# Kernel optimization log

Hardware: AMD Instinct MI355X
Metric: run time of the kernel (lower is better)

## Reference

```python
import jax, jax.numpy as jnp
import numpy as np

E = 256        # HP.EMBED_SIZE
R = 8          # number of derivation rules / MLPs
S = 512        # number of sequential derivation steps
N = 256        # nodes produced per step
N_INIT = 1024  # initial axiom (thax) embeddings
TOTAL = N_INIT + S * N  # 132096 rows in the vectors buffer
M = 65536      # masked nodes fed to eval_net


def setup_inputs() -> dict:
    key = jax.random.key(0)
    ks = jax.random.split(key, 12)
    rng = np.random.default_rng(0)

    init_vecs = jax.random.normal(ks[0], (N_INIT, E), jnp.float32)
    # rule MLPs: concat(2 parents) -> E (relu) -> E
    W1 = jax.random.normal(ks[1], (R, 2 * E, E), jnp.float32) * (1.0 / np.sqrt(2 * E))
    b1 = jnp.zeros((R, E), jnp.float32)
    W2 = jax.random.normal(ks[2], (R, E, E), jnp.float32) * (1.0 / np.sqrt(E))
    b2 = jnp.zeros((R, E), jnp.float32)
    # eval net: E -> E (relu) -> 1
    eval_W1 = jax.random.normal(ks[3], (E, E), jnp.float32) * (1.0 / np.sqrt(E))
    eval_b1 = jnp.zeros((E,), jnp.float32)
    eval_W2 = jax.random.normal(ks[4], (E, 1), jnp.float32) * (1.0 / np.sqrt(E))
    eval_b2 = jnp.zeros((1,), jnp.float32)

    # step s writes rows [N_INIT + s*N, N_INIT + (s+1)*N)
    ind_steps = (N_INIT + np.arange(S * N, dtype=np.int32)).reshape(S, N)
    # parents drawn causally from already-computed prefix [0, N_INIT + s*N)
    highs = (N_INIT + np.arange(S, dtype=np.int64) * N)[:, None, None]
    pars_ind_steps = (rng.random((S, N, 2)) * highs).astype(np.int32)
    rule_steps = rng.integers(0, R, size=(S,)).astype(np.int32)
    mask = rng.integers(0, TOTAL, size=(M,)).astype(np.int32)

    pos = jax.random.uniform(ks[5], (M,), jnp.float32)
    neg = jax.random.uniform(ks[6], (M,), jnp.float32)
    target = jnp.round(jax.random.uniform(ks[7], (M,), jnp.float32))

    return {
        'init_vecs': init_vecs, 'W1': W1, 'b1': b1, 'W2': W2, 'b2': b2,
        'eval_W1': eval_W1, 'eval_b1': eval_b1, 'eval_W2': eval_W2, 'eval_b2': eval_b2,
        'pos': pos, 'neg': neg, 'target': target,
        'ind_steps': jnp.asarray(ind_steps), 'pars_ind_steps': jnp.asarray(pars_ind_steps),
        'rule_steps': jnp.asarray(rule_steps), 'mask': jnp.asarray(mask),
    }


def reference(init_vecs, W1, b1, W2, b2, eval_W1, eval_b1, eval_W2, eval_b2,
              pos, neg, target, ind_steps, pars_ind_steps, rule_steps, mask):
    vectors = jnp.zeros((TOTAL, E), init_vecs.dtype).at[:N_INIT].set(init_vecs)

    def step(vec, xs):
        inds, pars, r = xs            # [N], [N,2], scalar rule id
        p = vec[pars].reshape(N, 2 * E)   # gather parents
        h = jax.nn.relu(p @ W1[r] + b1[r])
        out = h @ W2[r] + b2[r]
        return vec.at[inds].set(out), None  # scatter new node embeddings

    vectors, _ = jax.lax.scan(step, vectors, (ind_steps, pars_ind_steps, rule_steps))

    x = vectors[mask]
    val = (jax.nn.relu(x @ eval_W1 + eval_b1) @ eval_W2 + eval_b2)[:, 0]

    # pos_weight = POS_WEIGHT_EXTRA * tot_neg / tot_pos (constant w.r.t. grads)
    pw = jax.lax.stop_gradient(jnp.sum(neg) / jnp.maximum(jnp.sum(pos), 1.0))
    # BCEWithLogitsLoss(pos_weight, reduction='none')
    contrib = pw * target * jax.nn.softplus(-val) + (1.0 - target) * jax.nn.softplus(val)
    loss = jnp.sum((pos + neg) * contrib)
    posOK = jnp.sum(pos * (val >= 0))
    negOK = jnp.sum(neg * (val < 0))
    return loss, posOK, negOK
```

## Files before the change

### kernel.cpp

```cpp
#include <hip/hip_runtime.h>
#include <math.h>

#define EMB   256
#define TWOE  512
#define NINIT 1024
#define NSTEP 512
#define NPS   256
#define TOTAL (NINIT + NSTEP * NPS)
#define MM    65536
#define NNODE (NSTEP * NPS)
#define NKEY  2048
#define BTH   512
#define TROWS 64
#define CHK_SH  16384
#define RULE_SH (24 * CHK_SH)

typedef short s16x8 __attribute__((ext_vector_type(8)));
typedef float f32x4 __attribute__((ext_vector_type(4)));

#define OFF_VECH   0ull
#define OFF_VECL   ((size_t)TOTAL * EMB * 2)
#define OFF_VAL    (2ull * (size_t)TOTAL * EMB * 2)
#define OFF_CNT    (OFF_VAL + (size_t)MM * 4)
#define OFF_ACC    (OFF_CNT + 4096)
#define OFF_PW     (OFF_ACC + 64)
#define OFF_KCNT   (OFF_PW + 192)
#define OFF_KOFS   (OFF_KCNT + (size_t)NKEY * 4)
#define OFF_NL     (OFF_KOFS + (size_t)NKEY * 4)
#define OFF_BROWS  (OFF_NL + 256)
#define OFF_LVL8   (OFF_BROWS + (size_t)NNODE * 4)
#define OFF_WSPLIT (OFF_LVL8 + 132352)


__device__ __forceinline__ void store_dev_u32(unsigned* p, unsigned v) {
  asm volatile("global_store_dword %0, %1, off sc0 sc1" :: "v"(p), "v"(v) : "memory");
}
__device__ __forceinline__ void store_dev_b64(void* p, uint2 v) {
  asm volatile("global_store_dwordx2 %0, %1, off sc0 sc1" :: "v"(p), "v"(v) : "memory");
}
__device__ __forceinline__ void store_dev_b128(void* p, uint4 v) {
  store_dev_b64(p, make_uint2(v.x, v.y));
  store_dev_b64((char*)p + 8, make_uint2(v.z, v.w));
}
__device__ __forceinline__ unsigned load_dev_u32(const unsigned* p) {
  unsigned r;
  asm volatile("global_load_dword %0, %1, off sc0 sc1\n\ts_waitcnt vmcnt(0)"
               : "=v"(r) : "v"(p) : "memory");
  return r;
}

__device__ __forceinline__ void gbar_tree(unsigned* cnt, int xcd) {
  asm volatile("s_waitcnt vmcnt(0)" ::: "memory");
  __syncthreads();
  if (threadIdx.x == 0) {
    unsigned* xarr = cnt + 32 * xcd;
    unsigned* garr = cnt + 512;
    unsigned* gep  = cnt + 544;
    unsigned* xep  = cnt + 576 + 32 * xcd;
    unsigned o = __hip_atomic_fetch_add(xarr, 1u, __ATOMIC_RELAXED, __HIP_MEMORY_SCOPE_AGENT);
    unsigned tgt = o / 32u + 1u;
    if ((o & 31u) == 31u) {
      unsigned g = __hip_atomic_fetch_add(garr, 1u, __ATOMIC_RELAXED, __HIP_MEMORY_SCOPE_AGENT);
      unsigned gt = g / 8u + 1u;
      if ((g & 7u) == 7u) store_dev_u32(gep, gt);
      else while (load_dev_u32(gep) < gt) __builtin_amdgcn_s_sleep(1);
      store_dev_u32(xep, tgt);
    } else {
      while (load_dev_u32(xep) < tgt) __builtin_amdgcn_s_sleep(1);
    }
  }
  __syncthreads();
}

__device__ __forceinline__ void split8(const float* f, uint4& h4, uint4& l4) {
  unsigned hu[8], lu[8];
  #pragma unroll
  for (int i = 0; i < 8; ++i) {
    unsigned u = __builtin_bit_cast(unsigned, f[i]);
    float rh = __builtin_bit_cast(float, u & 0xffff0000u);
    float rl = f[i] - rh;
    hu[i] = u >> 16;
    lu[i] = __builtin_bit_cast(unsigned, rl) >> 16;
  }
  h4 = make_uint4(hu[0] | (hu[1] << 16), hu[2] | (hu[3] << 16),
                  hu[4] | (hu[5] << 16), hu[6] | (hu[7] << 16));
  l4 = make_uint4(lu[0] | (lu[1] << 16), lu[2] | (lu[3] << 16),
                  lu[4] | (lu[5] << 16), lu[6] | (lu[7] << 16));
}

__device__ __forceinline__ void stage_chunk(short* ldst, const short* gsrc,
                                            int w, int lane) {
  #pragma unroll
  for (int i = 0; i < 4; ++i) {
    int off = (w * 4 + i) * 512;
    __builtin_amdgcn_global_load_lds(
        (const __attribute__((address_space(1))) unsigned int*)(gsrc + off + lane * 8),
        (__attribute__((address_space(3))) unsigned int*)(ldst + off), 16, 0, 0);
  }
}

__global__ void zero_scratch(unsigned* cnt, double* acc) {
  for (int i = threadIdx.x; i < 1024; i += 256) cnt[i] = 0u;
  if (threadIdx.x < 8) acc[threadIdx.x] = 0.0;
}

__global__ void init_convert(const float* __restrict__ src,
                             unsigned short* __restrict__ vh,
                             unsigned short* __restrict__ vl) {
  int slot = blockIdx.x * blockDim.x + threadIdx.x;
  float f[8];
  *(float4*)&f[0] = reinterpret_cast<const float4*>(src)[slot * 2];
  *(float4*)&f[4] = reinterpret_cast<const float4*>(src)[slot * 2 + 1];
  uint4 h4, l4;
  split8(f, h4, l4);
  *(uint4*)(vh + (size_t)slot * 8) = h4;
  *(uint4*)(vl + (size_t)slot * 8) = l4;
}

__global__ __launch_bounds__(512)
void presplit(const float* __restrict__ W1, const float* __restrict__ W2,
              short* __restrict__ Ws)
{
  const int blk = blockIdx.x;
  const int r = blk / 24, c = blk % 24;
  const float* src; int kbase;
  if (c < 16) { src = W1 + (size_t)r * TWOE * EMB; kbase = c * 32; }
  else        { src = W2 + (size_t)r * EMB * EMB;  kbase = (c - 16) * 32; }
  short* dst = Ws + (size_t)blk * CHK_SH;
  const int tid = threadIdx.x;
  #pragma unroll
  for (int u = 0; u < 2; ++u) {
    int qq = tid + u * 512;
    int g = qq >> 6, l = qq & 63;
    const float* p = src + (size_t)(kbase + ((l >> 4) << 3)) * EMB + (g << 4) + (l & 15);
    float f[8];
    #pragma unroll
    for (int i = 0; i < 8; ++i) f[i] = p[i * EMB];
    uint4 h4, l4;
    split8(f, h4, l4);
    *(uint4*)(dst + (size_t)qq * 8) = h4;
    *(uint4*)(dst + 8192 + (size_t)qq * 8) = l4;
  }
}

__global__ __launch_bounds__(256)
void prepass_levels(const int* __restrict__ pars, unsigned char* __restrict__ lvl8,
                    int* __restrict__ nlp)
{
  __shared__ unsigned char slvl[TOTAL];
  __shared__ int swmax[4];
  const int t = threadIdx.x;
  for (int i = t; i < NINIT; i += 256) slvl[i] = 0;
  __syncthreads();
  int Pa[8], Pb[8];
  #pragma unroll
  for (int w = 0; w < 8; ++w) {
    Pa[w] = pars[2 * (w * NPS + t)];
    Pb[w] = pars[2 * (w * NPS + t) + 1];
  }
  int lmax = 0;
  for (int s0 = 0; s0 < NSTEP; s0 += 8) {
    int Na[8], Nb[8];
    if (s0 + 8 < NSTEP) {
      #pragma unroll
      for (int w = 0; w < 8; ++w) {
        Na[w] = pars[2 * ((s0 + 8 + w) * NPS + t)];
        Nb[w] = pars[2 * ((s0 + 8 + w) * NPS + t) + 1];
      }
    } else {
      #pragma unroll
      for (int w = 0; w < 8; ++w) { Na[w] = 0; Nb[w] = 0; }
    }
    #pragma unroll
    for (int w = 0; w < 8; ++w) {
      int l1 = slvl[Pa[w]], l2 = slvl[Pb[w]];
      int lv = 1 + (l1 > l2 ? l1 : l2);
      slvl[NINIT + (s0 + w) * NPS + t] = (unsigned char)lv;
      if (lv > lmax) lmax = lv;
      __syncthreads();
    }
    #pragma unroll
    for (int w = 0; w < 8; ++w) { Pa[w] = Na[w]; Pb[w] = Nb[w]; }
  }
  const unsigned* sv = (const unsigned*)slvl;
  unsigned* gv = (unsigned*)lvl8;
  for (int i = t; i < TOTAL / 4; i += 256) gv[i] = sv[i];
  for (int o = 32; o; o >>= 1) lmax = max(lmax, __shfl_down(lmax, o));
  if ((t & 63) == 0) swmax[t >> 6] = lmax;
  __syncthreads();
  if (t == 0) {
    int m = 0;
    for (int w = 0; w < 4; ++w) m = max(m, swmax[w]);
    nlp[0] = m;
  }
}

__global__ __launch_bounds__(1024)
void prepass_bucket(const unsigned char* __restrict__ lvl8, const int* __restrict__ rules,
                    int* __restrict__ kcnt, int* __restrict__ kofs,
                    int* __restrict__ brows)
{
  __shared__ int scnt[NKEY];
  __shared__ int sofs[NKEY];
  const int t = threadIdx.x;
  for (int k = t; k < NKEY; k += 1024) scnt[k] = 0;
  __syncthreads();
  for (int i = t; i < NNODE; i += 1024) {
    int key = (int)lvl8[NINIT + i] * 8 + rules[i >> 8];
    atomicAdd(&scnt[key], 1);
  }
  __syncthreads();
  if (t == 0) {
    int run = 0;
    for (int k = 0; k < NKEY; ++k) {
      sofs[k] = run; kofs[k] = run; kcnt[k] = scnt[k]; run += scnt[k];
    }
  }
  __syncthreads();
  for (int i = t; i < NNODE; i += 1024) {
    int key = (int)lvl8[NINIT + i] * 8 + rules[i >> 8];
    int pos = atomicAdd(&sofs[key], 1);
    brows[pos] = i;
  }
}

__global__ __launch_bounds__(BTH, 1)
void scan_kernel(const short* __restrict__ Ws, const float* __restrict__ b1,
                 const float* __restrict__ b2, const int* __restrict__ pars,
                 unsigned short* __restrict__ vech, unsigned short* __restrict__ vecl,
                 const int* __restrict__ kcnt, const int* __restrict__ kofs,
                 const int* __restrict__ brows, const int* __restrict__ nlp,
                 unsigned* __restrict__ cnt)
{
  __shared__ short wB[2][CHK_SH];
  __shared__ float hL[TROWS][260];
  __shared__ int spar[2 * TROWS];
  __shared__ int sorow[TROWS];
  const int tid = threadIdx.x;
  const int bid = blockIdx.x;
  const int lane = tid & 63;
  const int w = tid >> 6;
  const int rw = w & 1, cwb = (w >> 1) << 2;
  const int row16 = lane & 15, kb8 = (lane >> 4) << 3;
  const int arow0 = (rw << 5) + row16;
  const int arow1 = arow0 + 16;
  const int hrow = (rw << 5) + ((lane >> 4) << 2);
  const int NL = nlp[0];
  const int xcd = bid & 7, jb = bid >> 3;

  for (int lv = 1; lv <= NL; ++lv) {
    int cum[9]; cum[0] = 0;
    int cnts[8], ofss[8];
    #pragma unroll
    for (int r = 0; r < 8; ++r) {
      int c = kcnt[lv * 8 + r];
      cnts[r] = c; ofss[r] = kofs[lv * 8 + r];
      cum[r + 1] = cum[r] + ((c + TROWS - 1) >> 6);
    }
    const int G = cum[8];
    const int q = G >> 3, rm = G & 7;
    const int Gx = q + (xcd < rm ? 1 : 0);
    const int sx = xcd * q + (xcd < rm ? xcd : rm);
    for (int j = jb; j < Gx; j += 32) {
      const int g = sx + j;
      int rr = 0;
      while (g >= cum[rr + 1]) ++rr;
      const int t0 = g - cum[rr];
      const int cnt_b = cnts[rr], ofs_b = ofss[rr];
      const int tbase = t0 * TROWS;
      const short* __restrict__ Wr = Ws + (size_t)rr * RULE_SH;

      __syncthreads();
      stage_chunk(&wB[0][0], Wr, w, lane);
      if (tid < 2 * TROWS) {
        int slot = tbase + (tid >> 1);
        if (slot >= cnt_b) slot = cnt_b - 1;
        int node = brows[ofs_b + slot];
        spar[tid] = pars[2 * node + (tid & 1)];
        if ((tid & 1) == 0) sorow[tid >> 1] = NINIT + node;
      }
      __syncthreads();
      const int p00 = spar[2 * arow0], p01 = spar[2 * arow0 + 1];
      const int p10 = spar[2 * arow1], p11 = spar[2 * arow1 + 1];
      float b1v[4], b2v[4];
      #pragma unroll
      for (int g4 = 0; g4 < 4; ++g4) {
        b1v[g4] = b1[rr * EMB + ((cwb + g4) << 4) + row16];
        b2v[g4] = b2[rr * EMB + ((cwb + g4) << 4) + row16];
      }
      uint4 a0h, a0l, a1h, a1l;
      {
        size_t o0 = (size_t)p00 * EMB + kb8;
        size_t o1 = (size_t)p10 * EMB + kb8;
        a0h = *(const uint4*)(vech + o0); a0l = *(const uint4*)(vecl + o0);
        a1h = *(const uint4*)(vech + o1); a1l = *(const uint4*)(vecl + o1);
      }
      asm volatile("s_waitcnt vmcnt(0)" ::: "memory");
      __syncthreads();
      f32x4 acc0[4] = {{0,0,0,0},{0,0,0,0},{0,0,0,0},{0,0,0,0}};
      f32x4 acc1[4] = {{0,0,0,0},{0,0,0,0},{0,0,0,0},{0,0,0,0}};
      int cur = 0;
      #pragma unroll
      for (int c = 0; c < 16; ++c) {
        stage_chunk(&wB[cur ^ 1][0], Wr + (size_t)(c + 1) * CHK_SH, w, lane);
        uint4 n0h, n0l, n1h, n1l;
        if (c < 15) {
          int kg = (c + 1) * 32 + kb8;
          int q0 = (kg >> 8) ? p01 : p00;
          int q1 = (kg >> 8) ? p11 : p10;
          size_t o0 = (size_t)q0 * EMB + (kg & 255);
          size_t o1 = (size_t)q1 * EMB + (kg & 255);
          n0h = *(const uint4*)(vech + o0); n0l = *(const uint4*)(vecl + o0);
          n1h = *(const uint4*)(vech + o1); n1l = *(const uint4*)(vecl + o1);
        }
        s16x8 A0h = __builtin_bit_cast(s16x8, a0h);
        s16x8 A0l = __builtin_bit_cast(s16x8, a0l);
        s16x8 A1h = __builtin_bit_cast(s16x8, a1h);
        s16x8 A1l = __builtin_bit_cast(s16x8, a1l);
        #pragma unroll
        for (int g4 = 0; g4 < 4; ++g4) {
          const short* bp = &wB[cur][((cwb + g4) * 64 + lane) * 8];
          s16x8 Bh = *(const s16x8*)bp;
          s16x8 Bl = *(const s16x8*)(bp + 8192);
          acc0[g4] = __builtin_amdgcn_mfma_f32_16x16x32_bf16(A0h, Bh, acc0[g4], 0, 0, 0);
          acc0[g4] = __builtin_amdgcn_mfma_f32_16x16x32_bf16(A0h, Bl, acc0[g4], 0, 0, 0);
          acc0[g4] = __builtin_amdgcn_mfma_f32_16x16x32_bf16(A0l, Bh, acc0[g4], 0, 0, 0);
          acc1[g4] = __builtin_amdgcn_mfma_f32_16x16x32_bf16(A1h, Bh, acc1[g4], 0, 0, 0);
          acc1[g4] = __builtin_amdgcn_mfma_f32_16x16x32_bf16(A1h, Bl, acc1[g4], 0, 0, 0);
          acc1[g4] = __builtin_amdgcn_mfma_f32_16x16x32_bf16(A1l, Bh, acc1[g4], 0, 0, 0);
        }
        if (c == 15) {
          #pragma unroll
          for (int g4 = 0; g4 < 4; ++g4) {
            #pragma unroll
            for (int jj = 0; jj < 4; ++jj) {
              int col = ((cwb + g4) << 4) + row16;
              hL[hrow + jj][col]      = fmaxf(acc0[g4][jj] + b1v[g4], 0.f);
              hL[hrow + 16 + jj][col] = fmaxf(acc1[g4][jj] + b1v[g4], 0.f);
            }
          }
        }
        asm volatile("s_waitcnt vmcnt(0)" ::: "memory");
        __syncthreads();
        cur ^= 1;
        if (c < 15) { a0h = n0h; a0l = n0l; a1h = n1h; a1l = n1l; }
      }
      #pragma unroll
      for (int g4 = 0; g4 < 4; ++g4) {
        acc0[g4] = (f32x4){0, 0, 0, 0};
        acc1[g4] = (f32x4){0, 0, 0, 0};
      }
      #pragma unroll
      for (int c2 = 0; c2 < 8; ++c2) {
        if (c2 < 7)
          stage_chunk(&wB[cur ^ 1][0], Wr + (size_t)(17 + c2) * CHK_SH, w, lane);
        uint4 qh0, ql0, qh1, ql1;
        {
          float af[8];
          *(float4*)&af[0] = *(const float4*)&hL[arow0][c2 * 32 + kb8];
          *(float4*)&af[4] = *(const float4*)&hL[arow0][c2 * 32 + kb8 + 4];
          split8(af, qh0, ql0);
          *(float4*)&af[0] = *(const float4*)&hL[arow1][c2 * 32 + kb8];
          *(float4*)&af[4] = *(const float4*)&hL[arow1][c2 * 32 + kb8 + 4];
          split8(af, qh1, ql1);
        }
        s16x8 A0h = __builtin_bit_cast(s16x8, qh0);
        s16x8 A0l = __builtin_bit_cast(s16x8, ql0);
        s16x8 A1h = __builtin_bit_cast(s16x8, qh1);
        s16x8 A1l = __builtin_bit_cast(s16x8, ql1);
        #pragma unroll
        for (int g4 = 0; g4 < 4; ++g4) {
          const short* bp = &wB[cur][((cwb + g4) * 64 + lane) * 8];
          s16x8 Bh = *(const s16x8*)bp;
          s16x8 Bl = *(const s16x8*)(bp + 8192);
          acc0[g4] = __builtin_amdgcn_mfma_f32_16x16x32_bf16(A0h, Bh, acc0[g4], 0, 0, 0);
          acc0[g4] = __builtin_amdgcn_mfma_f32_16x16x32_bf16(A0h, Bl, acc0[g4], 0, 0, 0);
          acc0[g4] = __builtin_amdgcn_mfma_f32_16x16x32_bf16(A0l, Bh, acc0[g4], 0, 0, 0);
          acc1[g4] = __builtin_amdgcn_mfma_f32_16x16x32_bf16(A1h, Bh, acc1[g4], 0, 0, 0);
          acc1[g4] = __builtin_amdgcn_mfma_f32_16x16x32_bf16(A1h, Bl, acc1[g4], 0, 0, 0);
          acc1[g4] = __builtin_amdgcn_mfma_f32_16x16x32_bf16(A1l, Bh, acc1[g4], 0, 0, 0);
        }
        asm volatile("s_waitcnt vmcnt(0)" ::: "memory");
        __syncthreads();
        cur ^= 1;
      }
      #pragma unroll
      for (int g4 = 0; g4 < 4; ++g4) {
        #pragma unroll
        for (int jj = 0; jj < 4; ++jj) {
          int col = ((cwb + g4) << 4) + row16;
          hL[hrow + jj][col]      = acc0[g4][jj] + b2v[g4];
          hL[hrow + 16 + jj][col] = acc1[g4][jj] + b2v[g4];
        }
      }
      __syncthreads();
      #pragma unroll
      for (int u = 0; u < 4; ++u) {
        int s = tid + u * 512;
        int row = s >> 5, c8 = (s & 31) * 8;
        float of[8];
        *(float4*)&of[0] = *(const float4*)&hL[row][c8];
        *(float4*)&of[4] = *(const float4*)&hL[row][c8 + 4];
        uint4 h4, l4;
        split8(of, h4, l4);
        if (tbase + row < cnt_b) {
          size_t off = (size_t)sorow[row] * EMB + c8;
          store_dev_b128(vech + off, h4);
          store_dev_b128(vecl + off, l4);
        }
      }
    }
    gbar_tree(cnt, xcd);
  }
}

__global__ void reduce_pn(const float* __restrict__ pos, const float* __restrict__ neg,
                          double* acc) {
  double sp = 0.0, sn = 0.0;
  for (int m = blockIdx.x * blockDim.x + threadIdx.x; m < MM; m += gridDim.x * blockDim.x) {
    sp += (double)pos[m]; sn += (double)neg[m];
  }
  for (int o = 32; o; o >>= 1) { sp += __shfl_down(sp, o); sn += __shfl_down(sn, o); }
  __shared__ double rp[4], rn[4];
  int wid = threadIdx.x >> 6, lane = threadIdx.x & 63;
  if (lane == 0) { rp[wid] = sp; rn[wid] = sn; }
  __syncthreads();
  if (threadIdx.x == 0) {
    double tp = 0.0, tn = 0.0;
    for (int w = 0; w < 4; ++w) { tp += rp[w]; tn += rn[w]; }
    atomicAdd(&acc[0], tp); atomicAdd(&acc[1], tn);
  }
}

__global__ void pw_kernel(const double* __restrict__ acc, float* __restrict__ pw) {
  pw[0] = (float)(acc[1] / fmax(acc[0], 1.0));
}

__global__ __launch_bounds__(256)
void eval_kernel(const unsigned short* __restrict__ vh, const unsigned short* __restrict__ vl,
                 const int* __restrict__ mask,
                 const float* __restrict__ eW1, const float* __restrict__ eb1,
                 const float* __restrict__ eW2, const float* __restrict__ eb2,
                 float* __restrict__ val)
{
  __shared__ float xL[64][36];
  __shared__ float wLx[32][260];
  __shared__ int mrow[64];
  const int tid = threadIdx.x;
  const int a = tid >> 4, b = tid & 15;
  const int m0 = blockIdx.x * 64;
  if (tid < 64) mrow[tid] = mask[m0 + tid];
  __syncthreads();

  float acc[4][16];
  #pragma unroll
  for (int i = 0; i < 4; ++i)
    #pragma unroll
    for (int j = 0; j < 16; ++j) acc[i][j] = 0.f;

  for (int c = 0; c < 8; ++c) {
    const int e0 = c * 32;
    for (int idx = tid; idx < 64 * 4; idx += 256) {
      int rr = idx >> 2, u = idx & 3;
      size_t off = (size_t)mrow[rr] * EMB + e0 + u * 8;
      uint4 hv = *(const uint4*)(vh + off);
// ... 73 lines not shown
    float spn = fmaxf(-v, 0.f) + lp;
    float spp = fmaxf(v, 0.f) + lp;
    float contrib = pw * t * spn + (1.f - t) * spp;
    l += (double)((p + n) * contrib);
    if (v >= 0.f) pk += (double)p; else nk += (double)n;
  }
  for (int o = 32; o; o >>= 1) {
    l += __shfl_down(l, o); pk += __shfl_down(pk, o); nk += __shfl_down(nk, o);
  }
  __shared__ double s0[4], s1[4], s2[4];
  int wid = threadIdx.x >> 6, lane = threadIdx.x & 63;
  if (lane == 0) { s0[wid] = l; s1[wid] = pk; s2[wid] = nk; }
  __syncthreads();
  if (threadIdx.x == 0) {
    double ta = 0.0, tb = 0.0, tc = 0.0;
    for (int w = 0; w < 4; ++w) { ta += s0[w]; tb += s1[w]; tc += s2[w]; }
    atomicAdd(&acc[2], ta); atomicAdd(&acc[3], tb); atomicAdd(&acc[4], tc);
  }
}

__global__ void writeout(const double* __restrict__ acc, float* __restrict__ out) {
  if (threadIdx.x == 0) {
    out[0] = (float)acc[2];
    out[1] = (float)acc[3];
    out[2] = (float)acc[4];
  }
}

extern "C" void kernel_launch(void* const* d_in, const int* in_sizes, int n_in,
                              void* d_out, int out_size, void* d_ws, size_t ws_size,
                              hipStream_t stream)
{
  (void)in_sizes; (void)n_in; (void)out_size; (void)ws_size;
  const float* init_vecs = (const float*)d_in[0];
  const float* W1  = (const float*)d_in[1];
  const float* b1  = (const float*)d_in[2];
  const float* W2  = (const float*)d_in[3];
  const float* b2  = (const float*)d_in[4];
  const float* eW1 = (const float*)d_in[5];
  const float* eb1 = (const float*)d_in[6];
  const float* eW2 = (const float*)d_in[7];
  const float* eb2 = (const float*)d_in[8];
  const float* pos = (const float*)d_in[9];
  const float* neg = (const float*)d_in[10];
  const float* tgt = (const float*)d_in[11];
  const int* pars  = (const int*)d_in[13];
  const int* rules = (const int*)d_in[14];
  const int* mask  = (const int*)d_in[15];

  char* ws = (char*)d_ws;
  unsigned short* vech = (unsigned short*)(ws + OFF_VECH);
  unsigned short* vecl = (unsigned short*)(ws + OFF_VECL);
  float*    val   = (float*)(ws + OFF_VAL);
  unsigned* cnt   = (unsigned*)(ws + OFF_CNT);
  double*   acc   = (double*)(ws + OFF_ACC);
  float*    pw    = (float*)(ws + OFF_PW);
  int*      kcnt  = (int*)(ws + OFF_KCNT);
  int*      kofs  = (int*)(ws + OFF_KOFS);
  int*      nlp   = (int*)(ws + OFF_NL);
  int*      brows = (int*)(ws + OFF_BROWS);
  unsigned char* lvl8 = (unsigned char*)(ws + OFF_LVL8);
  short*    Ws    = (short*)(ws + OFF_WSPLIT);

  zero_scratch<<<1, 256, 0, stream>>>(cnt, acc);
  prepass_levels<<<1, 256, 0, stream>>>(pars, lvl8, nlp);
  prepass_bucket<<<1, 1024, 0, stream>>>(lvl8, rules, kcnt, kofs, brows);
  init_convert<<<128, 256, 0, stream>>>(init_vecs, vech, vecl);
  presplit<<<192, 512, 0, stream>>>(W1, W2, Ws);
  scan_kernel<<<256, BTH, 0, stream>>>(Ws, b1, b2, pars, vech, vecl,
                                       kcnt, kofs, brows, nlp, cnt);
  reduce_pn<<<128, 256, 0, stream>>>(pos, neg, acc);
  pw_kernel<<<1, 1, 0, stream>>>(acc, pw);
  eval_kernel<<<1024, 256, 0, stream>>>(vech, vecl, mask, eW1, eb1, eW2, eb2, val);
  loss_kernel<<<128, 256, 0, stream>>>(val, pos, neg, tgt, pw, acc);
  writeout<<<1, 1, 0, stream>>>(acc, (float*)d_out);
}
```

Measured before the change: 1.278 ms.

## Replace per-level grid barriers with per-tile dataflow readiness flags

The prepass now assigns each 64-row tile a global index, per-tile rule, offset and count, and records for every node which tile produces it. The scan kernel walks tiles in level order with a static stride and, before gathering, spins on the ready flags of the tiles that produced its parents, then sets its own flag after storing outputs. This removes the tree-structured grid barrier at every level so tiles can start as soon as their own dependencies are done. The cost is per-parent flag polling and reliance on the static tile order to avoid deadlock, since every block must be resident.

```diff
diff --git a/kernel.cpp b/kernel.cpp
--- a/kernel.cpp
+++ b/kernel.cpp
@@ -12,6 +12,7 @@
 #define NKEY  2048
 #define BTH   512
 #define TROWS 64
+#define MAXT  4096
 #define CHK_SH  16384
 #define RULE_SH (24 * CHK_SH)
 
@@ -29,7 +30,13 @@
 #define OFF_NL     (OFF_KOFS + (size_t)NKEY * 4)
 #define OFF_BROWS  (OFF_NL + 256)
 #define OFF_LVL8   (OFF_BROWS + (size_t)NNODE * 4)
-#define OFF_WSPLIT (OFF_LVL8 + 132352)
+#define OFF_PTILE  (OFF_LVL8 + 132352)
+#define OFF_TRUL   (OFF_PTILE + (size_t)NNODE * 4)
+#define OFF_TOFS   (OFF_TRUL + (size_t)MAXT * 4)
+#define OFF_TCNT   (OFF_TOFS + (size_t)MAXT * 4)
+#define OFF_FLAG   (OFF_TCNT + (size_t)MAXT * 4)
+#define OFF_NT     (OFF_FLAG + (size_t)MAXT * 4)
+#define OFF_WSPLIT (OFF_NT + 256)
 
 
 __device__ __forceinline__ void store_dev_u32(unsigned* p, unsigned v) {
@@ -47,29 +54,6 @@
   asm volatile("global_load_dword %0, %1, off sc0 sc1\n\ts_waitcnt vmcnt(0)"
                : "=v"(r) : "v"(p) : "memory");
   return r;
-}
-
-__device__ __forceinline__ void gbar_tree(unsigned* cnt, int xcd) {
-  asm volatile("s_waitcnt vmcnt(0)" ::: "memory");
-  __syncthreads();
-  if (threadIdx.x == 0) {
-    unsigned* xarr = cnt + 32 * xcd;
-    unsigned* garr = cnt + 512;
-    unsigned* gep  = cnt + 544;
-    unsigned* xep  = cnt + 576 + 32 * xcd;
-    unsigned o = __hip_atomic_fetch_add(xarr, 1u, __ATOMIC_RELAXED, __HIP_MEMORY_SCOPE_AGENT);
-    unsigned tgt = o / 32u + 1u;
-    if ((o & 31u) == 31u) {
-      unsigned g = __hip_atomic_fetch_add(garr, 1u, __ATOMIC_RELAXED, __HIP_MEMORY_SCOPE_AGENT);
-      unsigned gt = g / 8u + 1u;
-      if ((g & 7u) == 7u) store_dev_u32(gep, gt);
-      else while (load_dev_u32(gep) < gt) __builtin_amdgcn_s_sleep(1);
-      store_dev_u32(xep, tgt);
-    } else {
-      while (load_dev_u32(xep) < tgt) __builtin_amdgcn_s_sleep(1);
-    }
-  }
-  __syncthreads();
 }
 
 __device__ __forceinline__ void split8(const float* f, uint4& h4, uint4& l4) {
@@ -99,9 +83,10 @@
   }
 }
 
-__global__ void zero_scratch(unsigned* cnt, double* acc) {
-  for (int i = threadIdx.x; i < 1024; i += 256) cnt[i] = 0u;
-  if (threadIdx.x < 8) acc[threadIdx.x] = 0.0;
+__global__ void zero_scratch(unsigned* flags, double* acc) {
+  int i = blockIdx.x * 256 + threadIdx.x;
+  if (i < MAXT) flags[i] = 0u;
+  if (blockIdx.x == 0 && threadIdx.x < 8) acc[threadIdx.x] = 0.0;
 }
 
 __global__ void init_convert(const float* __restrict__ src,
@@ -198,10 +183,13 @@
 __global__ __launch_bounds__(1024)
 void prepass_bucket(const unsigned char* __restrict__ lvl8, const int* __restrict__ rules,
                     int* __restrict__ kcnt, int* __restrict__ kofs,
-                    int* __restrict__ brows)
+                    int* __restrict__ brows, int* __restrict__ ptile,
+                    int* __restrict__ trul, int* __restrict__ tofs,
+                    int* __restrict__ tcnt, int* __restrict__ ntp)
 {
   __shared__ int scnt[NKEY];
   __shared__ int sofs[NKEY];
+  __shared__ int stb[NKEY];
   const int t = threadIdx.x;
   for (int k = t; k < NKEY; k += 1024) scnt[k] = 0;
   __syncthreads();
@@ -211,16 +199,30 @@
   }
   __syncthreads();
   if (t == 0) {
-    int run = 0;
+    int run = 0, runt = 0;
     for (int k = 0; k < NKEY; ++k) {
-      sofs[k] = run; kofs[k] = run; kcnt[k] = scnt[k]; run += scnt[k];
-    }
+      sofs[k] = run; kofs[k] = run; kcnt[k] = scnt[k]; stb[k] = runt;
+      run += scnt[k];
+      runt += (scnt[k] + TROWS - 1) >> 6;
+    }
+    ntp[0] = runt;
   }
   __syncthreads();
   for (int i = t; i < NNODE; i += 1024) {
     int key = (int)lvl8[NINIT + i] * 8 + rules[i >> 8];
     int pos = atomicAdd(&sofs[key], 1);
     brows[pos] = i;
+    ptile[i] = stb[key] + ((pos - kofs[key]) >> 6);
+  }
+  for (int k = t; k < NKEY; k += 1024) {
+    int c = scnt[k];
+    if (c == 0) continue;
+    int tb = stb[k], ko = kofs[k];
+    for (int lt = 0; lt * TROWS < c; ++lt) {
+      trul[tb + lt] = k & 7;
+      tofs[tb + lt] = ko + lt * TROWS;
+      tcnt[tb + lt] = min(TROWS, c - lt * TROWS);
+    }
   }
 }
 
@@ -228,9 +230,10 @@
 void scan_kernel(const short* __restrict__ Ws, const float* __restrict__ b1,
                  const float* __restrict__ b2, const int* __restrict__ pars,
                  unsigned short* __restrict__ vech, unsigned short* __restrict__ vecl,
-                 const int* __restrict__ kcnt, const int* __restrict__ kofs,
-                 const int* __restrict__ brows, const int* __restrict__ nlp,
-                 unsigned* __restrict__ cnt)
+                 const int* __restrict__ brows, const int* __restrict__ ptile,
+                 const int* __restrict__ trul, const int* __restrict__ tofs,
+                 const int* __restrict__ tcnt, const int* __restrict__ ntp,
+                 unsigned* __restrict__ flags)
 {
   __shared__ short wB[2][CHK_SH];
   __shared__ float hL[TROWS][260];
@@ -245,172 +248,164 @@
   const int arow0 = (rw << 5) + row16;
   const int arow1 = arow0 + 16;
   const int hrow = (rw << 5) + ((lane >> 4) << 2);
-  const int NL = nlp[0];
-  const int xcd = bid & 7, jb = bid >> 3;
-
-  for (int lv = 1; lv <= NL; ++lv) {
-    int cum[9]; cum[0] = 0;
-    int cnts[8], ofss[8];
-    #pragma unroll
-    for (int r = 0; r < 8; ++r) {
-      int c = kcnt[lv * 8 + r];
-      cnts[r] = c; ofss[r] = kofs[lv * 8 + r];
-      cum[r + 1] = cum[r] + ((c + TROWS - 1) >> 6);
-    }
-    const int G = cum[8];
-    const int q = G >> 3, rm = G & 7;
-    const int Gx = q + (xcd < rm ? 1 : 0);
-    const int sx = xcd * q + (xcd < rm ? xcd : rm);
-    for (int j = jb; j < Gx; j += 32) {
-      const int g = sx + j;
-      int rr = 0;
-      while (g >= cum[rr + 1]) ++rr;
-      const int t0 = g - cum[rr];
-      const int cnt_b = cnts[rr], ofs_b = ofss[rr];
-      const int tbase = t0 * TROWS;
-      const short* __restrict__ Wr = Ws + (size_t)rr * RULE_SH;
-
-      __syncthreads();
-      stage_chunk(&wB[0][0], Wr, w, lane);
-      if (tid < 2 * TROWS) {
-        int slot = tbase + (tid >> 1);
-        if (slot >= cnt_b) slot = cnt_b - 1;
-        int node = brows[ofs_b + slot];
-        spar[tid] = pars[2 * node + (tid & 1)];
-        if ((tid & 1) == 0) sorow[tid >> 1] = NINIT + node;
-      }
-      __syncthreads();
-      const int p00 = spar[2 * arow0], p01 = spar[2 * arow0 + 1];
-      const int p10 = spar[2 * arow1], p11 = spar[2 * arow1 + 1];
-      float b1v[4], b2v[4];
+  const int NT = ntp[0];
+
+  for (int g = bid; g < NT; g += 256) {
+    const int rr = trul[g];
+    const int ofs = tofs[g];
+    const int cb = tcnt[g];
+    const short* __restrict__ Wr = Ws + (size_t)rr * RULE_SH;
+
+    __syncthreads();
+    stage_chunk(&wB[0][0], Wr, w, lane);
+    if (tid < 2 * TROWS) {
+      int slot = tid >> 1;
+      if (slot >= cb) slot = cb - 1;
+      int node = brows[ofs + slot];
+      spar[tid] = pars[2 * node + (tid & 1)];
+      if ((tid & 1) == 0) sorow[tid >> 1] = NINIT + node;
+    }
+    __syncthreads();
+    if (tid < 2 * TROWS) {
+      int p = spar[tid];
+      if (p >= NINIT) {
+        const unsigned* f = flags + ptile[p - NINIT];
+        while (load_dev_u32(f) == 0u) __builtin_amdgcn_s_sleep(1);
+      }
+    }
+    __syncthreads();
+    const int p00 = spar[2 * arow0], p01 = spar[2 * arow0 + 1];
+    const int p10 = spar[2 * arow1], p11 = spar[2 * arow1 + 1];
+    float b1v[4], b2v[4];
+    #pragma unroll
+    for (int g4 = 0; g4 < 4; ++g4) {
+      b1v[g4] = b1[rr * EMB + ((cwb + g4) << 4) + row16];
+      b2v[g4] = b2[rr * EMB + ((cwb + g4) << 4) + row16];
+    }
+    uint4 a0h, a0l, a1h, a1l;
+    {
+      size_t o0 = (size_t)p00 * EMB + kb8;
+      size_t o1 = (size_t)p10 * EMB + kb8;
+      a0h = *(const uint4*)(vech + o0); a0l = *(const uint4*)(vecl + o0);
+      a1h = *(const uint4*)(vech + o1); a1l = *(const uint4*)(vecl + o1);
+    }
+    asm volatile("s_waitcnt vmcnt(0)" ::: "memory");
+    __syncthreads();
+    f32x4 acc0[4] = {{0,0,0,0},{0,0,0,0},{0,0,0,0},{0,0,0,0}};
+    f32x4 acc1[4] = {{0,0,0,0},{0,0,0,0},{0,0,0,0},{0,0,0,0}};
+    int cur = 0;
+    #pragma unroll
+    for (int c = 0; c < 16; ++c) {
+      stage_chunk(&wB[cur ^ 1][0], Wr + (size_t)(c + 1) * CHK_SH, w, lane);
+      uint4 n0h, n0l, n1h, n1l;
+      if (c < 15) {
+        int kg = (c + 1) * 32 + kb8;
+        int q0 = (kg >> 8) ? p01 : p00;
+        int q1 = (kg >> 8) ? p11 : p10;
+        size_t o0 = (size_t)q0 * EMB + (kg & 255);
+        size_t o1 = (size_t)q1 * EMB + (kg & 255);
+        n0h = *(const uint4*)(vech + o0); n0l = *(const uint4*)(vecl + o0);
+        n1h = *(const uint4*)(vech + o1); n1l = *(const uint4*)(vecl + o1);
+      }
+      s16x8 A0h = __builtin_bit_cast(s16x8, a0h);
+      s16x8 A0l = __builtin_bit_cast(s16x8, a0l);
+      s16x8 A1h = __builtin_bit_cast(s16x8, a1h);
+      s16x8 A1l = __builtin_bit_cast(s16x8, a1l);
       #pragma unroll
       for (int g4 = 0; g4 < 4; ++g4) {
-        b1v[g4] = b1[rr * EMB + ((cwb + g4) << 4) + row16];
-        b2v[g4] = b2[rr * EMB + ((cwb + g4) << 4) + row16];
-      }
-      uint4 a0h, a0l, a1h, a1l;
-      {
-        size_t o0 = (size_t)p00 * EMB + kb8;
-        size_t o1 = (size_t)p10 * EMB + kb8;
-        a0h = *(const uint4*)(vech + o0); a0l = *(const uint4*)(vecl + o0);
-        a1h = *(const uint4*)(vech + o1); a1l = *(const uint4*)(vecl + o1);
+        const short* bp = &wB[cur][((cwb + g4) * 64 + lane) * 8];
+        s16x8 Bh = *(const s16x8*)bp;
+        s16x8 Bl = *(const s16x8*)(bp + 8192);
+        acc0[g4] = __builtin_amdgcn_mfma_f32_16x16x32_bf16(A0h, Bh, acc0[g4], 0, 0, 0);
+        acc0[g4] = __builtin_amdgcn_mfma_f32_16x16x32_bf16(A0h, Bl, acc0[g4], 0, 0, 0);
+        acc0[g4] = __builtin_amdgcn_mfma_f32_16x16x32_bf16(A0l, Bh, acc0[g4], 0, 0, 0);
+        acc1[g4] = __builtin_amdgcn_mfma_f32_16x16x32_bf16(A1h, Bh, acc1[g4], 0, 0, 0);
+        acc1[g4] = __builtin_amdgcn_mfma_f32_16x16x32_bf16(A1h, Bl, acc1[g4], 0, 0, 0);
+        acc1[g4] = __builtin_amdgcn_mfma_f32_16x16x32_bf16(A1l, Bh, acc1[g4], 0, 0, 0);
+      }
+      if (c == 15) {
+        #pragma unroll
+        for (int g4 = 0; g4 < 4; ++g4) {
+          #pragma unroll
+          for (int jj = 0; jj < 4; ++jj) {
+            int col = ((cwb + g4) << 4) + row16;
+            hL[hrow + jj][col]      = fmaxf(acc0[g4][jj] + b1v[g4], 0.f);
+            hL[hrow + 16 + jj][col] = fmaxf(acc1[g4][jj] + b1v[g4], 0.f);
+          }
+        }
       }
       asm volatile("s_waitcnt vmcnt(0)" ::: "memory");
       __syncthreads();
-      f32x4 acc0[4] = {{0,0,0,0},{0,0,0,0},{0,0,0,0},{0,0,0,0}};
-      f32x4 acc1[4] = {{0,0,0,0},{0,0,0,0},{0,0,0,0},{0,0,0,0}};
-      int cur = 0;
-      #pragma unroll
-      for (int c = 0; c < 16; ++c) {
-        stage_chunk(&wB[cur ^ 1][0], Wr + (size_t)(c + 1) * CHK_SH, w, lane);
-        uint4 n0h, n0l, n1h, n1l;
-        if (c < 15) {
-          int kg = (c + 1) * 32 + kb8;
-          int q0 = (kg >> 8) ? p01 : p00;
-          int q1 = (kg >> 8) ? p11 : p10;
-          size_t o0 = (size_t)q0 * EMB + (kg & 255);
-          size_t o1 = (size_t)q1 * EMB + (kg & 255);
-          n0h = *(const uint4*)(vech + o0); n0l = *(const uint4*)(vecl + o0);
-          n1h = *(const uint4*)(vech + o1); n1l = *(const uint4*)(vecl + o1);
-        }
-        s16x8 A0h = __builtin_bit_cast(s16x8, a0h);
-        s16x8 A0l = __builtin_bit_cast(s16x8, a0l);
-        s16x8 A1h = __builtin_bit_cast(s16x8, a1h);
-        s16x8 A1l = __builtin_bit_cast(s16x8, a1l);
-        #pragma unroll
-        for (int g4 = 0; g4 < 4; ++g4) {
-          const short* bp = &wB[cur][((cwb + g4) * 64 + lane) * 8];
-          s16x8 Bh = *(const s16x8*)bp;
-          s16x8 Bl = *(const s16x8*)(bp + 8192);
-          acc0[g4] = __builtin_amdgcn_mfma_f32_16x16x32_bf16(A0h, Bh, acc0[g4], 0, 0, 0);
-          acc0[g4] = __builtin_amdgcn_mfma_f32_16x16x32_bf16(A0h, Bl, acc0[g4], 0, 0, 0);
-          acc0[g4] = __builtin_amdgcn_mfma_f32_16x16x32_bf16(A0l, Bh, acc0[g4], 0, 0, 0);
-          acc1[g4] = __builtin_amdgcn_mfma_f32_16x16x32_bf16(A1h, Bh, acc1[g4], 0, 0, 0);
-          acc1[g4] = __builtin_amdgcn_mfma_f32_16x16x32_bf16(A1h, Bl, acc1[g4], 0, 0, 0);
-          acc1[g4] = __builtin_amdgcn_mfma_f32_16x16x32_bf16(A1l, Bh, acc1[g4], 0, 0, 0);
-        }
-        if (c == 15) {
-          #pragma unroll
-          for (int g4 = 0; g4 < 4; ++g4) {
-            #pragma unroll
-            for (int jj = 0; jj < 4; ++jj) {
-              int col = ((cwb + g4) << 4) + row16;
-              hL[hrow + jj][col]      = fmaxf(acc0[g4][jj] + b1v[g4], 0.f);
-              hL[hrow + 16 + jj][col] = fmaxf(acc1[g4][jj] + b1v[g4], 0.f);
-            }
-          }
-        }
-        asm volatile("s_waitcnt vmcnt(0)" ::: "memory");
-        __syncthreads();
-        cur ^= 1;
-        if (c < 15) { a0h = n0h; a0l = n0l; a1h = n1h; a1l = n1l; }
-      }
+      cur ^= 1;
+      if (c < 15) { a0h = n0h; a0l = n0l; a1h = n1h; a1l = n1l; }
+    }
+    #pragma unroll
+    for (int g4 = 0; g4 < 4; ++g4) {
+      acc0[g4] = (f32x4){0, 0, 0, 0};
+      acc1[g4] = (f32x4){0, 0, 0, 0};
+    }
+    #pragma unroll
+    for (int c2 = 0; c2 < 8; ++c2) {
+      if (c2 < 7)
+        stage_chunk(&wB[cur ^ 1][0], Wr + (size_t)(17 + c2) * CHK_SH, w, lane);
+      uint4 qh0, ql0, qh1, ql1;
+      {
+        float af[8];
+        *(float4*)&af[0] = *(const float4*)&hL[arow0][c2 * 32 + kb8];
+        *(float4*)&af[4] = *(const float4*)&hL[arow0][c2 * 32 + kb8 + 4];
+        split8(af, qh0, ql0);
+        *(float4*)&af[0] = *(const float4*)&hL[arow1][c2 * 32 + kb8];
+        *(float4*)&af[4] = *(const float4*)&hL[arow1][c2 * 32 + kb8 + 4];
+        split8(af, qh1, ql1);
+      }
+      s16x8 A0h = __builtin_bit_cast(s16x8, qh0);
+      s16x8 A0l = __builtin_bit_cast(s16x8, ql0);
+      s16x8 A1h = __builtin_bit_cast(s16x8, qh1);
+      s16x8 A1l = __builtin_bit_cast(s16x8, ql1);
       #pragma unroll
       for (int g4 = 0; g4 < 4; ++g4) {
-        acc0[g4] = (f32x4){0, 0, 0, 0};
-        acc1[g4] = (f32x4){0, 0, 0, 0};
-      }
-      #pragma unroll
-      for (int c2 = 0; c2 < 8; ++c2) {
-        if (c2 < 7)
-          stage_chunk(&wB[cur ^ 1][0], Wr + (size_t)(17 + c2) * CHK_SH, w, lane);
-        uint4 qh0, ql0, qh1, ql1;
-        {
-          float af[8];
-          *(float4*)&af[0] = *(const float4*)&hL[arow0][c2 * 32 + kb8];
-          *(float4*)&af[4] = *(const float4*)&hL[arow0][c2 * 32 + kb8 + 4];
-          split8(af, qh0, ql0);
-          *(float4*)&af[0] = *(const float4*)&hL[arow1][c2 * 32 + kb8];
-          *(float4*)&af[4] = *(const float4*)&hL[arow1][c2 * 32 + kb8 + 4];
-          split8(af, qh1, ql1);
-        }
-        s16x8 A0h = __builtin_bit_cast(s16x8, qh0);
-        s16x8 A0l = __builtin_bit_cast(s16x8, ql0);
-        s16x8 A1h = __builtin_bit_cast(s16x8, qh1);
-        s16x8 A1l = __builtin_bit_cast(s16x8, ql1);
-        #pragma unroll
-        for (int g4 = 0; g4 < 4; ++g4) {
-          const short* bp = &wB[cur][((cwb + g4) * 64 + lane) * 8];
-          s16x8 Bh = *(const s16x8*)bp;
-          s16x8 Bl = *(const s16x8*)(bp + 8192);
-          acc0[g4] = __builtin_amdgcn_mfma_f32_16x16x32_bf16(A0h, Bh, acc0[g4], 0, 0, 0);
-          acc0[g4] = __builtin_amdgcn_mfma_f32_16x16x32_bf16(A0h, Bl, acc0[g4], 0, 0, 0);
-          acc0[g4] = __builtin_amdgcn_mfma_f32_16x16x32_bf16(A0l, Bh, acc0[g4], 0, 0, 0);
-          acc1[g4] = __builtin_amdgcn_mfma_f32_16x16x32_bf16(A1h, Bh, acc1[g4], 0, 0, 0);
-          acc1[g4] = __builtin_amdgcn_mfma_f32_16x16x32_bf16(A1h, Bl, acc1[g4], 0, 0, 0);
-          acc1[g4] = __builtin_amdgcn_mfma_f32_16x16x32_bf16(A1l, Bh, acc1[g4], 0, 0, 0);
-        }
-        asm volatile("s_waitcnt vmcnt(0)" ::: "memory");
-        __syncthreads();
-        cur ^= 1;
-      }
-      #pragma unroll
-      for (int g4 = 0; g4 < 4; ++g4) {
-        #pragma unroll
-        for (int jj = 0; jj < 4; ++jj) {
-          int col = ((cwb + g4) << 4) + row16;
-          hL[hrow + jj][col]      = acc0[g4][jj] + b2v[g4];
-          hL[hrow + 16 + jj][col] = acc1[g4][jj] + b2v[g4];
-        }
-      }
+        const short* bp = &wB[cur][((cwb + g4) * 64 + lane) * 8];
+        s16x8 Bh = *(const s16x8*)bp;
+        s16x8 Bl = *(const s16x8*)(bp + 8192);
+        acc0[g4] = __builtin_amdgcn_mfma_f32_16x16x32_bf16(A0h, Bh, acc0[g4], 0, 0, 0);
+        acc0[g4] = __builtin_amdgcn_mfma_f32_16x16x32_bf16(A0h, Bl, acc0[g4], 0, 0, 0);
+        acc0[g4] = __builtin_amdgcn_mfma_f32_16x16x32_bf16(A0l, Bh, acc0[g4], 0, 0, 0);
+        acc1[g4] = __builtin_amdgcn_mfma_f32_16x16x32_bf16(A1h, Bh, acc1[g4], 0, 0, 0);
+        acc1[g4] = __builtin_amdgcn_mfma_f32_16x16x32_bf16(A1h, Bl, acc1[g4], 0, 0, 0);
+        acc1[g4] = __builtin_amdgcn_mfma_f32_16x16x32_bf16(A1l, Bh, acc1[g4], 0, 0, 0);
+      }
+      asm volatile("s_waitcnt vmcnt(0)" ::: "memory");
       __syncthreads();
-      #pragma unroll
-      for (int u = 0; u < 4; ++u) {
-        int s = tid + u * 512;
-        int row = s >> 5, c8 = (s & 31) * 8;
-        float of[8];
-        *(float4*)&of[0] = *(const float4*)&hL[row][c8];
-        *(float4*)&of[4] = *(const float4*)&hL[row][c8 + 4];
-        uint4 h4, l4;
-        split8(of, h4, l4);
-        if (tbase + row < cnt_b) {
-          size_t off = (size_t)sorow[row] * EMB + c8;
-          store_dev_b128(vech + off, h4);
-          store_dev_b128(vecl + off, l4);
-        }
-      }
-    }
-    gbar_tree(cnt, xcd);
+      cur ^= 1;
+    }
+    #pragma unroll
+    for (int g4 = 0; g4 < 4; ++g4) {
+      #pragma unroll
+      for (int jj = 0; jj < 4; ++jj) {
+        int col = ((cwb + g4) << 4) + row16;
+        hL[hrow + jj][col]      = acc0[g4][jj] + b2v[g4];
+        hL[hrow + 16 + jj][col] = acc1[g4][jj] + b2v[g4];
+      }
+    }
+    __syncthreads();
+    #pragma unroll
+    for (int u = 0; u < 4; ++u) {
+      int s = tid + u * 512;
+      int row = s >> 5, c8 = (s & 31) * 8;
+      float of[8];
+      *(float4*)&of[0] = *(const float4*)&hL[row][c8];
+      *(float4*)&of[4] = *(const float4*)&hL[row][c8 + 4];
+      uint4 h4, l4;
+      split8(of, h4, l4);
+      if (row < cb) {
+        size_t off = (size_t)sorow[row] * EMB + c8;
+        store_dev_b128(vech + off, h4);
+        store_dev_b128(vecl + off, l4);
+      }
+    }
+    asm volatile("s_waitcnt vmcnt(0)" ::: "memory");
+    __syncthreads();
+    if (tid == 0) store_dev_u32(flags + g, 1u);
   }
 }
 
@@ -590,7 +585,6 @@
   unsigned short* vech = (unsigned short*)(ws + OFF_VECH);
   unsigned short* vecl = (unsigned short*)(ws + OFF_VECL);
   float*    val   = (float*)(ws + OFF_VAL);
-  unsigned* cnt   = (unsigned*)(ws + OFF_CNT);
   double*   acc   = (double*)(ws + OFF_ACC);
   float*    pw    = (float*)(ws + OFF_PW);
   int*      kcnt  = (int*)(ws + OFF_KCNT);
@@ -598,15 +592,22 @@
   int*      nlp   = (int*)(ws + OFF_NL);
   int*      brows = (int*)(ws + OFF_BROWS);
   unsigned char* lvl8 = (unsigned char*)(ws + OFF_LVL8);
+  int*      ptile = (int*)(ws + OFF_PTILE);
+  int*      trul  = (int*)(ws + OFF_TRUL);
+  int*      tofs  = (int*)(ws + OFF_TOFS);
+  int*      tcnt  = (int*)(ws + OFF_TCNT);
+  unsigned* flags = (unsigned*)(ws + OFF_FLAG);
+  int*      ntp   = (int*)(ws + OFF_NT);
   short*    Ws    = (short*)(ws + OFF_WSPLIT);
 
-  zero_scratch<<<1, 256, 0, stream>>>(cnt, acc);
+  zero_scratch<<<16, 256, 0, stream>>>(flags, acc);
   prepass_levels<<<1, 256, 0, stream>>>(pars, lvl8, nlp);
-  prepass_bucket<<<1, 1024, 0, stream>>>(lvl8, rules, kcnt, kofs, brows);
+  prepass_bucket<<<1, 1024, 0, stream>>>(lvl8, rules, kcnt, kofs, brows,
+                                         ptile, trul, tofs, tcnt, ntp);
   init_convert<<<128, 256, 0, stream>>>(init_vecs, vech, vecl);
   presplit<<<192, 512, 0, stream>>>(W1, W2, Ws);
   scan_kernel<<<256, BTH, 0, stream>>>(Ws, b1, b2, pars, vech, vecl,
-                                       kcnt, kofs, brows, nlp, cnt);
+                                       brows, ptile, trul, tofs, tcnt, ntp, flags);
   reduce_pn<<<128, 256, 0, stream>>>(pos, neg, acc);
   pw_kernel<<<1, 1, 0, stream>>>(acc, pw);
   eval_kernel<<<1024, 256, 0, stream>>>(vech, vecl, mask, eW1, eb1, eW2, eb2, val);
```

Result: slower. 1.347 ms (+5.4%).

## Replace grid barrier with per-level done counters and pin rules to blocks

Applied to the files above, without the earlier changes.

Replaces the tree grid barrier between dependency levels with per-level completion counters: each block waits only until the previous level's tile count is reached, then works on its own tiles. Each block's rule is now fixed by its block index mod 8, so biases load once and tiles are no longer balanced across rules at each level. The hidden activations are also stored in shared memory already split into bf16 hi/lo halves, so the second GEMM and the writeback no longer re-split them. The risks are load imbalance when one rule has many more tiles at a level, and a spin on a single counter per level.

```diff
diff --git a/kernel.cpp b/kernel.cpp
--- a/kernel.cpp
+++ b/kernel.cpp
@@ -29,7 +29,8 @@
 #define OFF_NL     (OFF_KOFS + (size_t)NKEY * 4)
 #define OFF_BROWS  (OFF_NL + 256)
 #define OFF_LVL8   (OFF_BROWS + (size_t)NNODE * 4)
-#define OFF_WSPLIT (OFF_LVL8 + 132352)
+#define OFF_TPL    (OFF_LVL8 + 132352)
+#define OFF_WSPLIT (OFF_TPL + 4096)
 
 
 __device__ __forceinline__ void store_dev_u32(unsigned* p, unsigned v) {
@@ -47,29 +48,6 @@
   asm volatile("global_load_dword %0, %1, off sc0 sc1\n\ts_waitcnt vmcnt(0)"
                : "=v"(r) : "v"(p) : "memory");
   return r;
-}
-
-__device__ __forceinline__ void gbar_tree(unsigned* cnt, int xcd) {
-  asm volatile("s_waitcnt vmcnt(0)" ::: "memory");
-  __syncthreads();
-  if (threadIdx.x == 0) {
-    unsigned* xarr = cnt + 32 * xcd;
-    unsigned* garr = cnt + 512;
-    unsigned* gep  = cnt + 544;
-    unsigned* xep  = cnt + 576 + 32 * xcd;
-    unsigned o = __hip_atomic_fetch_add(xarr, 1u, __ATOMIC_RELAXED, __HIP_MEMORY_SCOPE_AGENT);
-    unsigned tgt = o / 32u + 1u;
-    if ((o & 31u) == 31u) {
-      unsigned g = __hip_atomic_fetch_add(garr, 1u, __ATOMIC_RELAXED, __HIP_MEMORY_SCOPE_AGENT);
-      unsigned gt = g / 8u + 1u;
-      if ((g & 7u) == 7u) store_dev_u32(gep, gt);
-      else while (load_dev_u32(gep) < gt) __builtin_amdgcn_s_sleep(1);
-      store_dev_u32(xep, tgt);
-    } else {
-      while (load_dev_u32(xep) < tgt) __builtin_amdgcn_s_sleep(1);
-    }
-  }
-  __syncthreads();
 }
 
 __device__ __forceinline__ void split8(const float* f, uint4& h4, uint4& l4) {
@@ -88,6 +66,14 @@
                   lu[4] | (lu[5] << 16), lu[6] | (lu[7] << 16));
 }
 
+__device__ __forceinline__ void split1(float f, short& hi, short& lo) {
+  unsigned u = __builtin_bit_cast(unsigned, f);
+  float rh = __builtin_bit_cast(float, u & 0xffff0000u);
+  float rl = f - rh;
+  hi = (short)(u >> 16);
+  lo = (short)(__builtin_bit_cast(unsigned, rl) >> 16);
+}
+
 __device__ __forceinline__ void stage_chunk(short* ldst, const short* gsrc,
                                             int w, int lane) {
   #pragma unroll
@@ -99,8 +85,8 @@
   }
 }
 
-__global__ void zero_scratch(unsigned* cnt, double* acc) {
-  for (int i = threadIdx.x; i < 1024; i += 256) cnt[i] = 0u;
+__global__ void zero_scratch(unsigned* done, double* acc) {
+  if (threadIdx.x < 256) done[threadIdx.x] = 0u;
   if (threadIdx.x < 8) acc[threadIdx.x] = 0.0;
 }
 
@@ -198,7 +184,7 @@
 __global__ __launch_bounds__(1024)
 void prepass_bucket(const unsigned char* __restrict__ lvl8, const int* __restrict__ rules,
                     int* __restrict__ kcnt, int* __restrict__ kofs,
-                    int* __restrict__ brows)
+                    int* __restrict__ brows, int* __restrict__ tpl)
 {
   __shared__ int scnt[NKEY];
   __shared__ int sofs[NKEY];
@@ -216,6 +202,12 @@
       sofs[k] = run; kofs[k] = run; kcnt[k] = scnt[k]; run += scnt[k];
     }
   }
+  if (t < 256) {
+    int s = 0;
+    #pragma unroll
+    for (int r = 0; r < 8; ++r) s += (scnt[t * 8 + r] + TROWS - 1) >> 6;
+    tpl[t] = s;
+  }
   __syncthreads();
   for (int i = t; i < NNODE; i += 1024) {
     int key = (int)lvl8[NINIT + i] * 8 + rules[i >> 8];
@@ -229,11 +221,12 @@
                  const float* __restrict__ b2, const int* __restrict__ pars,
                  unsigned short* __restrict__ vech, unsigned short* __restrict__ vecl,
                  const int* __restrict__ kcnt, const int* __restrict__ kofs,
-                 const int* __restrict__ brows, const int* __restrict__ nlp,
-                 unsigned* __restrict__ cnt)
+                 const int* __restrict__ brows, const int* __restrict__ tpl,
+                 const int* __restrict__ nlp, unsigned* __restrict__ done)
 {
   __shared__ short wB[2][CHK_SH];
-  __shared__ float hL[TROWS][260];
+  __shared__ short hH[TROWS][264];
+  __shared__ short hLo[TROWS][264];
   __shared__ int spar[2 * TROWS];
   __shared__ int sorow[TROWS];
   const int tid = threadIdx.x;
@@ -245,49 +238,42 @@
   const int arow0 = (rw << 5) + row16;
   const int arow1 = arow0 + 16;
   const int hrow = (rw << 5) + ((lane >> 4) << 2);
+  const int x = bid & 7;
+  const int slot = bid >> 3;
+  const short* __restrict__ Wr = Ws + (size_t)x * RULE_SH;
   const int NL = nlp[0];
-  const int xcd = bid & 7, jb = bid >> 3;
+  float b1v[4], b2v[4];
+  #pragma unroll
+  for (int g4 = 0; g4 < 4; ++g4) {
+    b1v[g4] = b1[x * EMB + ((cwb + g4) << 4) + row16];
+    b2v[g4] = b2[x * EMB + ((cwb + g4) << 4) + row16];
+  }
 
   for (int lv = 1; lv <= NL; ++lv) {
-    int cum[9]; cum[0] = 0;
-    int cnts[8], ofss[8];
-    #pragma unroll
-    for (int r = 0; r < 8; ++r) {
-      int c = kcnt[lv * 8 + r];
-      cnts[r] = c; ofss[r] = kofs[lv * 8 + r];
-      cum[r + 1] = cum[r] + ((c + TROWS - 1) >> 6);
-    }
-    const int G = cum[8];
-    const int q = G >> 3, rm = G & 7;
-    const int Gx = q + (xcd < rm ? 1 : 0);
-    const int sx = xcd * q + (xcd < rm ? xcd : rm);
-    for (int j = jb; j < Gx; j += 32) {
-      const int g = sx + j;
-      int rr = 0;
-      while (g >= cum[rr + 1]) ++rr;
-      const int t0 = g - cum[rr];
-      const int cnt_b = cnts[rr], ofs_b = ofss[rr];
-      const int tbase = t0 * TROWS;
-      const short* __restrict__ Wr = Ws + (size_t)rr * RULE_SH;
-
-      __syncthreads();
+    const int k = lv * 8 + x;
+    const int ck = kcnt[k], ok = kofs[k];
+    const int nt = (ck + TROWS - 1) >> 6;
+    if (tid == 0 && lv > 1) {
+      const unsigned need = (unsigned)tpl[lv - 1];
+      const unsigned* dp = done + (lv - 1);
+      while (load_dev_u32(dp) < need) __builtin_amdgcn_s_sleep(2);
+    }
+    __syncthreads();
+    for (int j = slot; j < nt; j += 32) {
+      const int ofs = ok + j * TROWS;
+      const int cb = min(TROWS, ck - j * TROWS);
+
       stage_chunk(&wB[0][0], Wr, w, lane);
       if (tid < 2 * TROWS) {
-        int slot = tbase + (tid >> 1);
-        if (slot >= cnt_b) slot = cnt_b - 1;
-        int node = brows[ofs_b + slot];
+        int slotr = tid >> 1;
+        if (slotr >= cb) slotr = cb - 1;
+        int node = brows[ofs + slotr];
         spar[tid] = pars[2 * node + (tid & 1)];
         if ((tid & 1) == 0) sorow[tid >> 1] = NINIT + node;
       }
       __syncthreads();
       const int p00 = spar[2 * arow0], p01 = spar[2 * arow0 + 1];
       const int p10 = spar[2 * arow1], p11 = spar[2 * arow1 + 1];
-      float b1v[4], b2v[4];
-      #pragma unroll
-      for (int g4 = 0; g4 < 4; ++g4) {
-        b1v[g4] = b1[rr * EMB + ((cwb + g4) << 4) + row16];
-        b2v[g4] = b2[rr * EMB + ((cwb + g4) << 4) + row16];
-      }
       uint4 a0h, a0l, a1h, a1l;
       {
         size_t o0 = (size_t)p00 * EMB + kb8;
@@ -335,8 +321,11 @@
             #pragma unroll
             for (int jj = 0; jj < 4; ++jj) {
               int col = ((cwb + g4) << 4) + row16;
-              hL[hrow + jj][col]      = fmaxf(acc0[g4][jj] + b1v[g4], 0.f);
-              hL[hrow + 16 + jj][col] = fmaxf(acc1[g4][jj] + b1v[g4], 0.f);
+              short hi, lo;
+              split1(fmaxf(acc0[g4][jj] + b1v[g4], 0.f), hi, lo);
+              hH[hrow + jj][col] = hi; hLo[hrow + jj][col] = lo;
+              split1(fmaxf(acc1[g4][jj] + b1v[g4], 0.f), hi, lo);
+              hH[hrow + 16 + jj][col] = hi; hLo[hrow + 16 + jj][col] = lo;
             }
           }
         }
@@ -354,20 +343,11 @@
       for (int c2 = 0; c2 < 8; ++c2) {
         if (c2 < 7)
           stage_chunk(&wB[cur ^ 1][0], Wr + (size_t)(17 + c2) * CHK_SH, w, lane);
-        uint4 qh0, ql0, qh1, ql1;
-        {
-          float af[8];
-          *(float4*)&af[0] = *(const float4*)&hL[arow0][c2 * 32 + kb8];
-          *(float4*)&af[4] = *(const float4*)&hL[arow0][c2 * 32 + kb8 + 4];
-          split8(af, qh0, ql0);
-          *(float4*)&af[0] = *(const float4*)&hL[arow1][c2 * 32 + kb8];
-          *(float4*)&af[4] = *(const float4*)&hL[arow1][c2 * 32 + kb8 + 4];
-          split8(af, qh1, ql1);
-        }
-        s16x8 A0h = __builtin_bit_cast(s16x8, qh0);
-        s16x8 A0l = __builtin_bit_cast(s16x8, ql0);
-        s16x8 A1h = __builtin_bit_cast(s16x8, qh1);
-        s16x8 A1l = __builtin_bit_cast(s16x8, ql1);
+        const int kc = c2 * 32 + kb8;
+        s16x8 A0h = *(const s16x8*)&hH[arow0][kc];
+        s16x8 A0l = *(const s16x8*)&hLo[arow0][kc];
+        s16x8 A1h = *(const s16x8*)&hH[arow1][kc];
+        s16x8 A1l = *(const s16x8*)&hLo[arow1][kc];
         #pragma unroll
         for (int g4 = 0; g4 < 4; ++g4) {
           const short* bp = &wB[cur][((cwb + g4) * 64 + lane) * 8];
@@ -389,8 +369,11 @@
         #pragma unroll
         for (int jj = 0; jj < 4; ++jj) {
           int col = ((cwb + g4) << 4) + row16;
-          hL[hrow + jj][col]      = acc0[g4][jj] + b2v[g4];
-          hL[hrow + 16 + jj][col] = acc1[g4][jj] + b2v[g4];
+          short hi, lo;
+          split1(acc0[g4][jj] + b2v[g4], hi, lo);
+          hH[hrow + jj][col] = hi; hLo[hrow + jj][col] = lo;
+          split1(acc1[g4][jj] + b2v[g4], hi, lo);
+          hH[hrow + 16 + jj][col] = hi; hLo[hrow + 16 + jj][col] = lo;
         }
       }
       __syncthreads();
@@ -398,19 +381,20 @@
       for (int u = 0; u < 4; ++u) {
         int s = tid + u * 512;
         int row = s >> 5, c8 = (s & 31) * 8;
-        float of[8];
-        *(float4*)&of[0] = *(const float4*)&hL[row][c8];
-        *(float4*)&of[4] = *(const float4*)&hL[row][c8 + 4];
-        uint4 h4, l4;
-        split8(of, h4, l4);
-        if (tbase + row < cnt_b) {
+        uint4 h4 = *(const uint4*)&hH[row][c8];
+        uint4 l4 = *(const uint4*)&hLo[row][c8];
+        if (row < cb) {
           size_t off = (size_t)sorow[row] * EMB + c8;
           store_dev_b128(vech + off, h4);
           store_dev_b128(vecl + off, l4);
         }
       }
-    }
-    gbar_tree(cnt, xcd);
+      asm volatile("s_waitcnt vmcnt(0)" ::: "memory");
+      __syncthreads();
+      if (tid == 0)
+        __hip_atomic_fetch_add(done + lv, 1u, __ATOMIC_RELAXED, __HIP_MEMORY_SCOPE_AGENT);
+      __syncthreads();
+    }
   }
 }
 
@@ -590,7 +574,7 @@
   unsigned short* vech = (unsigned short*)(ws + OFF_VECH);
   unsigned short* vecl = (unsigned short*)(ws + OFF_VECL);
   float*    val   = (float*)(ws + OFF_VAL);
-  unsigned* cnt   = (unsigned*)(ws + OFF_CNT);
+  unsigned* done  = (unsigned*)(ws + OFF_CNT);
   double*   acc   = (double*)(ws + OFF_ACC);
   float*    pw    = (float*)(ws + OFF_PW);
   int*      kcnt  = (int*)(ws + OFF_KCNT);
@@ -598,15 +582,16 @@
   int*      nlp   = (int*)(ws + OFF_NL);
   int*      brows = (int*)(ws + OFF_BROWS);
   unsigned char* lvl8 = (unsigned char*)(ws + OFF_LVL8);
+  int*      tpl   = (int*)(ws + OFF_TPL);
   short*    Ws    = (short*)(ws + OFF_WSPLIT);
 
-  zero_scratch<<<1, 256, 0, stream>>>(cnt, acc);
+  zero_scratch<<<1, 256, 0, stream>>>(done, acc);
   prepass_levels<<<1, 256, 0, stream>>>(pars, lvl8, nlp);
-  prepass_bucket<<<1, 1024, 0, stream>>>(lvl8, rules, kcnt, kofs, brows);
+  prepass_bucket<<<1, 1024, 0, stream>>>(lvl8, rules, kcnt, kofs, brows, tpl);
   init_convert<<<128, 256, 0, stream>>>(init_vecs, vech, vecl);
   presplit<<<192, 512, 0, stream>>>(W1, W2, Ws);
   scan_kernel<<<256, BTH, 0, stream>>>(Ws, b1, b2, pars, vech, vecl,
-                                       kcnt, kofs, brows, nlp, cnt);
+                                       kcnt, kofs, brows, tpl, nlp, done);
   reduce_pn<<<128, 256, 0, stream>>>(pos, neg, acc);
   pw_kernel<<<1, 1, 0, stream>>>(acc, pw);
   eval_kernel<<<1024, 256, 0, stream>>>(vech, vecl, mask, eW1, eb1, eW2, eb2, val);
```

After: 1.626 ms. 27.2% more time.
